# Kernel tuning notes

Hardware: AMD Instinct MI355X
Metric: run time of the kernel (lower is better)

Reference implementation:

```python
import jax, jax.numpy as jnp
import numpy as np

ROPE_BASE = 10000.0

def rotate_half(x):
    d = x.shape[-1] // 2
    return jnp.concatenate([-x[..., d:], x[..., :d]], axis=-1)

def rope_cos_sin(seq_len, head_dim, dtype=jnp.float32):
    inv_freq = 1.0 / (ROPE_BASE ** (jnp.arange(0, head_dim, 2, dtype=jnp.float32) / head_dim))
    t = jnp.arange(seq_len, dtype=jnp.float32)
    freqs = jnp.outer(t, inv_freq)              # [T, hd/2]
    emb = jnp.concatenate([freqs, freqs], axis=-1)  # [T, hd]
    return jnp.cos(emb).astype(dtype), jnp.sin(emb).astype(dtype)

def alibi_slopes(num_heads):
    return jnp.asarray([2.0 ** (-8.0 * i / num_heads) for i in range(1, num_heads + 1)], dtype=jnp.float32)

def setup_inputs() -> dict:
    key = jax.random.key(0)
    k1, k2, k3 = jax.random.split(key, 3)
    B, T, H = 2, 2048, 1024
    return {
        "q": jax.random.normal(k1, (B, T, H), dtype=jnp.float32),
        "k": jax.random.normal(k2, (B, T, H), dtype=jnp.float32),
        "v": jax.random.normal(k3, (B, T, H), dtype=jnp.float32),
        "num_heads": 16,
    }

def reference(q, k, v, num_heads):
    B, T, H = q.shape
    nh = num_heads
    hd = H // nh
    q = q.reshape(B, T, nh, hd)
    k = k.reshape(B, T, nh, hd)
    v = v.reshape(B, T, nh, hd)
    cos, sin = rope_cos_sin(T, hd, q.dtype)      # [T, hd]
    cos = cos[None, :, None, :]                  # [1, T, 1, hd]
    sin = sin[None, :, None, :]
    q = q * cos + rotate_half(q) * sin
    k = k * cos + rotate_half(k) * sin
    # ALiBi additive bias: [nh, T, T]
    rel = jnp.arange(T)[None, :] - jnp.arange(T)[:, None]   # memory - context
    bias = alibi_slopes(nh)[:, None, None] * rel.astype(q.dtype)
    scale = 1.0 / jnp.sqrt(jnp.asarray(hd, dtype=q.dtype))
    scores = jnp.einsum('bqhd,bkhd->bhqk', q, k) * scale + bias[None]
    attn = jax.nn.softmax(scores, axis=-1)
    out = jnp.einsum('bhqk,bkhd->bqhd', attn, v)
    return out.reshape(B, T, H)
```

## Files before the change

### kernel.cpp

```cpp
#include <hip/hip_runtime.h>
#include <math.h>

#define TB 2
#define TT 2048
#define NH 16
#define HD 64
#define HSZ 1024

typedef float floatx4 __attribute__((ext_vector_type(4)));
typedef __bf16 bf16x4 __attribute__((ext_vector_type(4)));
typedef __bf16 bf16x8 __attribute__((ext_vector_type(8)));

#define LOG2E  1.4426950408889634f
#define NEGF   (-0.4152410118609203f)
#define INV2PI 0.15915494309189535f

__global__ __launch_bounds__(256)
void prep_kernel(const float* __restrict__ K, const float* __restrict__ V,
                 __bf16* __restrict__ Kp, __bf16* __restrict__ Vp) {
    int blk = blockIdx.x;
    int kt = blk & 31;
    int bh = blk >> 5;
    int b = bh >> 4, h = bh & 15;
    int tid = threadIdx.x;

    {
        int key = tid >> 2, qq = tid & 3;
        int tglob = kt * 64 + key;
        const float* krow = K + ((size_t)(b * TT + tglob)) * HSZ + h * HD + qq * 8;
        float x0[8], x1[8];
        *(floatx4*)&x0[0] = *(const floatx4*)&krow[0];
        *(floatx4*)&x0[4] = *(const floatx4*)&krow[4];
        *(floatx4*)&x1[0] = *(const floatx4*)&krow[32];
        *(floatx4*)&x1[4] = *(const floatx4*)&krow[36];
        bf16x8 y0, y1;
        #pragma unroll
        for (int j = 0; j < 8; ++j) {
            float freq = exp2f((float)(qq * 8 + j) * NEGF);
            float rv = (float)tglob * freq * INV2PI;
            rv -= floorf(rv);
            float s = __builtin_amdgcn_sinf(rv);
            float c = __builtin_amdgcn_cosf(rv);
            y0[j] = (__bf16)(x0[j] * c - x1[j] * s);
            y1[j] = (__bf16)(x1[j] * c + x0[j] * s);
        }
        size_t base = ((size_t)blk * 4 + (key & 3)) * 1024 + (size_t)(qq * 16 + (key >> 2)) * 8;
        *(bf16x8*)(Kp + base)       = y0;
        *(bf16x8*)(Kp + base + 512) = y1;
    }

    __shared__ __bf16 lt[64][72];
    {
        int vkey = tid >> 2, dg = (tid & 3) * 16;
        const float* vrow = V + ((size_t)(b * TT + kt * 64 + vkey)) * HSZ + h * HD + dg;
        floatx4 v0 = *(const floatx4*)&vrow[0];
        floatx4 v1 = *(const floatx4*)&vrow[4];
        floatx4 v2 = *(const floatx4*)&vrow[8];
        floatx4 v3 = *(const floatx4*)&vrow[12];
        #pragma unroll
        for (int j = 0; j < 4; ++j) {
            lt[dg + j][vkey]      = (__bf16)v0[j];
            lt[dg + 4 + j][vkey]  = (__bf16)v1[j];
            lt[dg + 8 + j][vkey]  = (__bf16)v2[j];
            lt[dg + 12 + j][vkey] = (__bf16)v3[j];
        }
    }
    __syncthreads();
    #pragma unroll
    for (int ss = 0; ss < 2; ++ss) {
        int s = tid + ss * 256;
        int hg = s >> 6;
        int l = s & 63;
        int lq = l >> 4, lr = l & 15;
        int h2 = hg >> 2, g = hg & 3;
        bf16x8 o = *(const bf16x8*)&lt[g * 16 + lr][h2 * 32 + lq * 8];
        *(bf16x8*)(Vp + (size_t)blk * 4096 + (size_t)hg * 512 + (size_t)l * 8) = o;
    }
}

__global__ __launch_bounds__(256, 2)
void attn_kernel(const float* __restrict__ Q, const __bf16* __restrict__ Kp,
                 const __bf16* __restrict__ Vp, float* __restrict__ Out) {
    int blk0 = blockIdx.x;
    int rank = blk0 >> 5;
    int h = (rank < 5) ? (11 + rank) : (15 - rank);
    int rest = blk0 & 31;
    int b = rest >> 4;
    int qb = rest & 15;
    int bh = b * 16 + h;
    int tid = threadIdx.x;
    int wave = tid >> 6, lane = tid & 63;
    int lane15 = lane & 15, quad = lane >> 4;

    __shared__ __align__(16) __bf16 sP[4][2][16][72];

    const float scale2 = 0.125f * LOG2E;
    const float slope2 = exp2f(-0.5f * (float)(h + 1)) * LOG2E;
    const float ms     = slope2 * 2047.0f + 20.0f;

    int nkt = (int)(41.58f * exp2f(0.5f * (float)(h + 1)) * (1.0f / 64.0f)) + 2;
    if (nkt > 32) nkt = 32;
    const int kt_beg = 32 - nkt;

    int qbase = qb * 128 + wave * 32;
    int d0 = quad * 8;
    bf16x8 aQ0[2], aQ1[2];
    #pragma unroll
    for (int qf = 0; qf < 2; ++qf) {
        int t_q = qbase + qf * 16 + lane15;
        const float* qrow = Q + ((size_t)(b * TT + t_q) * HSZ) + h * HD;
        float q0[8], q1[8];
        *(floatx4*)&q0[0] = *(const floatx4*)&qrow[d0];
        *(floatx4*)&q0[4] = *(const floatx4*)&qrow[d0 + 4];
        *(floatx4*)&q1[0] = *(const floatx4*)&qrow[d0 + 32];
        *(floatx4*)&q1[4] = *(const floatx4*)&qrow[d0 + 36];
        #pragma unroll
        for (int j = 0; j < 8; ++j) {
            float freq = exp2f((float)(d0 + j) * NEGF);
            float rv = (float)t_q * freq * INV2PI;
            rv -= floorf(rv);
            float sn = __builtin_amdgcn_sinf(rv);
            float cs = __builtin_amdgcn_cosf(rv);
            aQ0[qf][j] = (__bf16)((q0[j] * cs - q1[j] * sn) * scale2);
            aQ1[qf][j] = (__bf16)((q1[j] * cs + q0[j] * sn) * scale2);
        }
    }

    float slk2[4];
    #pragma unroll
    for (int nt = 0; nt < 4; ++nt)
        slk2[nt] = slope2 * (float)(4 * lane15 + nt) - ms;
    const float dstep = slope2 * 64.0f;

    floatx4 O[2][4];
    float lrow[2][4];
    #pragma unroll
    for (int qf = 0; qf < 2; ++qf)
        #pragma unroll
        for (int r = 0; r < 4; ++r) {
            O[qf][r] = (floatx4){0.f, 0.f, 0.f, 0.f};
            lrow[qf][r] = 0.f;
        }

    const __bf16* Kb = Kp + (size_t)bh * (TT * HD) + (size_t)lane * 8;
    const __bf16* Vb = Vp + (size_t)bh * (TT * HD) + (size_t)lane * 8;

    const int kt1 = TT / 64;

    bf16x8 bk[4][2];
    {
        const __bf16* kbase = Kb + (size_t)kt_beg * 4096;
        #pragma unroll
        for (int nt = 0; nt < 4; ++nt) {
            bk[nt][0] = *(const bf16x8*)(kbase + nt * 1024);
            bk[nt][1] = *(const bf16x8*)(kbase + nt * 1024 + 512);
        }
    }

    #pragma unroll 1
    for (int kt = kt_beg; kt < kt1; ++kt) {
        const __bf16* vbase = Vb + (size_t)kt * 4096;
        bf16x8 bv[2][4];
        #pragma unroll
        for (int hg = 0; hg < 8; ++hg)
            bv[hg >> 2][hg & 3] = *(const bf16x8*)(vbase + hg * 512);

        float biask = dstep * (float)kt;
        #pragma unroll
        for (int qf = 0; qf < 2; ++qf) {
            float P[4][4];
            #pragma unroll
            for (int nt = 0; nt < 4; ++nt) {
                floatx4 acc = {0.f, 0.f, 0.f, 0.f};
                acc = __builtin_amdgcn_mfma_f32_16x16x32_bf16(aQ0[qf], bk[nt][0], acc, 0, 0, 0);
                acc = __builtin_amdgcn_mfma_f32_16x16x32_bf16(aQ1[qf], bk[nt][1], acc, 0, 0, 0);
                float bias = slk2[nt] + biask;
                #pragma unroll
                for (int r = 0; r < 4; ++r)
                    P[nt][r] = __builtin_amdgcn_exp2f(acc[r] + bias);
            }
            #pragma unroll
            for (int r = 0; r < 4; ++r) {
                lrow[qf][r] += (P[0][r] + P[1][r]) + (P[2][r] + P[3][r]);
                bf16x4 pp;
                pp[0] = (__bf16)P[0][r]; pp[1] = (__bf16)P[1][r];
                pp[2] = (__bf16)P[2][r]; pp[3] = (__bf16)P[3][r];
                *(bf16x4*)&sP[wave][qf][quad * 4 + r][4 * lane15] = pp;
            }
        }

        if (kt + 1 < kt1) {
            const __bf16* kbase = Kb + (size_t)(kt + 1) * 4096;
            #pragma unroll
            for (int nt = 0; nt < 4; ++nt) {
                bk[nt][0] = *(const bf16x8*)(kbase + nt * 1024);
                bk[nt][1] = *(const bf16x8*)(kbase + nt * 1024 + 512);
            }
        }

        #pragma unroll
        for (int qf = 0; qf < 2; ++qf) {
            #pragma unroll
            for (int h2 = 0; h2 < 2; ++h2) {
                bf16x8 aP = *(const bf16x8*)&sP[wave][qf][lane15][h2 * 32 + quad * 8];
                O[qf][0] = __builtin_amdgcn_mfma_f32_16x16x32_bf16(aP, bv[h2][0], O[qf][0], 0, 0, 0);
                O[qf][1] = __builtin_amdgcn_mfma_f32_16x16x32_bf16(aP, bv[h2][1], O[qf][1], 0, 0, 0);
                O[qf][2] = __builtin_amdgcn_mfma_f32_16x16x32_bf16(aP, bv[h2][2], O[qf][2], 0, 0, 0);
                O[qf][3] = __builtin_amdgcn_mfma_f32_16x16x32_bf16(aP, bv[h2][3], O[qf][3], 0, 0, 0);
            }
        }
    }

    #pragma unroll
    for (int qf = 0; qf < 2; ++qf) {
        #pragma unroll
        for (int r = 0; r < 4; ++r) {
            float l = lrow[qf][r];
            l += __shfl_xor(l, 1);
            l += __shfl_xor(l, 2);
            l += __shfl_xor(l, 4);
            l += __shfl_xor(l, 8);
            float inv = 1.0f / l;
            int t = qbase + qf * 16 + quad * 4 + r;
            size_t base = ((size_t)(b * TT + t)) * HSZ + h * HD + lane15;
            Out[base +  0] = O[qf][0][r] * inv;
            Out[base + 16] = O[qf][1][r] * inv;
            Out[base + 32] = O[qf][2][r] * inv;
            Out[base + 48] = O[qf][3][r] * inv;
        }
    }
}

extern "C" void kernel_launch(void* const* d_in, const int* in_sizes, int n_in,
                              void* d_out, int out_size, void* d_ws, size_t ws_size,
                              hipStream_t stream) {
    const float* q = (const float*)d_in[0];
    const float* k = (const float*)d_in[1];
    const float* v = (const float*)d_in[2];
    float* out = (float*)d_out;

    char* ws = (char*)d_ws;
    __bf16* Kp = (__bf16*)ws;
    __bf16* Vp = (__bf16*)(ws + (size_t)8 * 1024 * 1024);

    prep_kernel<<<dim3(TB * NH * (TT / 64)), 256, 0, stream>>>(k, v, Kp, Vp);
    attn_kernel<<<dim3(TB * NH * 16), 256, 0, stream>>>(q, Kp, Vp, out);
}
```

Baseline: 127.3 us.

## Software-pipeline attention loop: overlap PV of previous tile with QK of next

Restructures the key-tile loop into a two-stage software pipeline. The P·V MFMAs of tile kt-1 are interleaved with the QK/exp of tile kt, using double-buffered V registers and a double-buffered shared P tile, with the loop unrolled by two. The goal is to hide V load latency and the LDS round trip, and to give the scheduler independent MFMA and exp work to overlap. In exchange it raises register pressure (two V register sets) and doubles the shared memory used for P, which could hurt occupancy at the 2-blocks-per-SM launch bound.

```diff
diff --git a/kernel.cpp b/kernel.cpp
--- a/kernel.cpp
+++ b/kernel.cpp
@@ -92,7 +92,7 @@
     int wave = tid >> 6, lane = tid & 63;
     int lane15 = lane & 15, quad = lane >> 4;
 
-    __shared__ __align__(16) __bf16 sP[4][2][16][72];
+    __shared__ __align__(16) __bf16 sP[2][4][2][16][72];
 
     const float scale2 = 0.125f * LOG2E;
     const float slope2 = exp2f(-0.5f * (float)(h + 1)) * LOG2E;
@@ -145,26 +145,25 @@
     const __bf16* Kb = Kp + (size_t)bh * (TT * HD) + (size_t)lane * 8;
     const __bf16* Vb = Vp + (size_t)bh * (TT * HD) + (size_t)lane * 8;
 
-    const int kt1 = TT / 64;
-
     bf16x8 bk[4][2];
-    {
-        const __bf16* kbase = Kb + (size_t)kt_beg * 4096;
+    bf16x8 bvA[2][4], bvB[2][4];
+
+    auto load_bk = [&](int kt_) {
+        const __bf16* kb = Kb + (size_t)kt_ * 4096;
         #pragma unroll
         for (int nt = 0; nt < 4; ++nt) {
-            bk[nt][0] = *(const bf16x8*)(kbase + nt * 1024);
-            bk[nt][1] = *(const bf16x8*)(kbase + nt * 1024 + 512);
-        }
-    }
-
-    #pragma unroll 1
-    for (int kt = kt_beg; kt < kt1; ++kt) {
-        const __bf16* vbase = Vb + (size_t)kt * 4096;
-        bf16x8 bv[2][4];
+            bk[nt][0] = *(const bf16x8*)(kb + nt * 1024);
+            bk[nt][1] = *(const bf16x8*)(kb + nt * 1024 + 512);
+        }
+    };
+    auto load_bv = [&](bf16x8 (&bvt)[2][4], int kt_) {
+        const __bf16* vb = Vb + (size_t)kt_ * 4096;
         #pragma unroll
         for (int hg = 0; hg < 8; ++hg)
-            bv[hg >> 2][hg & 3] = *(const bf16x8*)(vbase + hg * 512);
-
+            bvt[hg >> 2][hg & 3] = *(const bf16x8*)(vb + hg * 512);
+    };
+
+    auto qk_phase = [&](int kt, int sb) {
         float biask = dstep * (float)kt;
         #pragma unroll
         for (int qf = 0; qf < 2; ++qf) {
@@ -185,30 +184,51 @@
                 bf16x4 pp;
                 pp[0] = (__bf16)P[0][r]; pp[1] = (__bf16)P[1][r];
                 pp[2] = (__bf16)P[2][r]; pp[3] = (__bf16)P[3][r];
-                *(bf16x4*)&sP[wave][qf][quad * 4 + r][4 * lane15] = pp;
+                *(bf16x4*)&sP[sb][wave][qf][quad * 4 + r][4 * lane15] = pp;
             }
         }
-
-        if (kt + 1 < kt1) {
-            const __bf16* kbase = Kb + (size_t)(kt + 1) * 4096;
-            #pragma unroll
-            for (int nt = 0; nt < 4; ++nt) {
-                bk[nt][0] = *(const bf16x8*)(kbase + nt * 1024);
-                bk[nt][1] = *(const bf16x8*)(kbase + nt * 1024 + 512);
-            }
-        }
-
+    };
+
+    auto pv_phase = [&](bf16x8 (&bvt)[2][4], int sb) {
         #pragma unroll
         for (int qf = 0; qf < 2; ++qf) {
             #pragma unroll
             for (int h2 = 0; h2 < 2; ++h2) {
-                bf16x8 aP = *(const bf16x8*)&sP[wave][qf][lane15][h2 * 32 + quad * 8];
-                O[qf][0] = __builtin_amdgcn_mfma_f32_16x16x32_bf16(aP, bv[h2][0], O[qf][0], 0, 0, 0);
-                O[qf][1] = __builtin_amdgcn_mfma_f32_16x16x32_bf16(aP, bv[h2][1], O[qf][1], 0, 0, 0);
-                O[qf][2] = __builtin_amdgcn_mfma_f32_16x16x32_bf16(aP, bv[h2][2], O[qf][2], 0, 0, 0);
-                O[qf][3] = __builtin_amdgcn_mfma_f32_16x16x32_bf16(aP, bv[h2][3], O[qf][3], 0, 0, 0);
+                bf16x8 aP = *(const bf16x8*)&sP[sb][wave][qf][lane15][h2 * 32 + quad * 8];
+                O[qf][0] = __builtin_amdgcn_mfma_f32_16x16x32_bf16(aP, bvt[h2][0], O[qf][0], 0, 0, 0);
+                O[qf][1] = __builtin_amdgcn_mfma_f32_16x16x32_bf16(aP, bvt[h2][1], O[qf][1], 0, 0, 0);
+                O[qf][2] = __builtin_amdgcn_mfma_f32_16x16x32_bf16(aP, bvt[h2][2], O[qf][2], 0, 0, 0);
+                O[qf][3] = __builtin_amdgcn_mfma_f32_16x16x32_bf16(aP, bvt[h2][3], O[qf][3], 0, 0, 0);
             }
         }
+    };
+
+    load_bk(kt_beg);
+    load_bv(bvA, kt_beg);
+    qk_phase(kt_beg, 0);
+    if (kt_beg + 1 < 32) load_bk(kt_beg + 1);
+
+    const int N = 32 - kt_beg - 1;
+    int kt = kt_beg + 1;
+    #pragma unroll 1
+    for (int i = 0; i + 1 < N; i += 2) {
+        load_bv(bvB, kt);
+        pv_phase(bvA, 0);
+        qk_phase(kt, 1);
+        if (kt + 1 < 32) load_bk(kt + 1);
+        load_bv(bvA, kt + 1);
+        pv_phase(bvB, 1);
+        qk_phase(kt + 1, 0);
+        if (kt + 2 < 32) load_bk(kt + 2);
+        kt += 2;
+    }
+    if (N & 1) {
+        load_bv(bvB, kt);
+        pv_phase(bvA, 0);
+        qk_phase(kt, 1);
+        pv_phase(bvB, 1);
+    } else {
+        pv_phase(bvA, 0);
     }
 
     #pragma unroll
```

New measurement: 125.7 us. Within noise of the previous version (-1.2%).
